# Performance work log

Measured on AMD Instinct MI355X. Metric: run time of the kernel, lower is better.

The kernel has to match this reference:

```python
import jax, jax.numpy as jnp
import numpy as np

D_OUT = 64  # out_embed_size, also the softmax scale base

def setup_inputs() -> dict:
    key = jax.random.key(0)
    kx, kk, kq, kv = jax.random.split(key, 4)
    B, T, C = 8, 2048, 768
    x = jax.random.normal(kx, (B, T, C), dtype=jnp.float32)
    # torch Linear weights are [out, in]; store as [in, out] for x @ W
    s = 1.0 / np.sqrt(C)
    Wk = jax.random.uniform(kk, (C, D_OUT), jnp.float32, -s, s)
    Wq = jax.random.uniform(kq, (C, D_OUT), jnp.float32, -s, s)
    Wv = jax.random.uniform(kv, (C, D_OUT), jnp.float32, -s, s)
    return {"x": x, "Wq": Wq, "Wk": Wk, "Wv": Wv}

def reference(x, Wq, Wk, Wv):
    B, T, C = x.shape
    q = x @ Wq  # [B,T,D]
    k = x @ Wk
    v = x @ Wv
    scale = D_OUT ** -0.5
    qk = jnp.einsum('btd,bsd->bts', q, k) * scale  # [B,T,T]
    causal = jnp.tril(jnp.ones((T, T), dtype=bool))
    qk = jnp.where(causal, qk, -jnp.inf)
    attn = jax.nn.softmax(qk, axis=-1)
    # dropout p=0.0 -> identity
    return jnp.einsum('bts,bsd->btd', attn, v)
```

## Files before the change

### kernel.cpp

```cpp
#include <hip/hip_runtime.h>
#include <hip/hip_bf16.h>

#define BB 8
#define TT 2048
#define CC 768
#define DD 64
#define BT (BB * TT)

typedef __attribute__((ext_vector_type(8))) short bf16x8;
typedef __attribute__((ext_vector_type(4))) float f32x4;

__device__ __forceinline__ unsigned short f2b(float f) {
  unsigned u = __builtin_bit_cast(unsigned, f);
  u += 0x7fffu + ((u >> 16) & 1u);
  return (unsigned short)(u >> 16);
}

__device__ __forceinline__ bf16x8 pack8(float4 a, float4 b) {
  unsigned short t[8] = {f2b(a.x), f2b(a.y), f2b(a.z), f2b(a.w),
                         f2b(b.x), f2b(b.y), f2b(b.z), f2b(b.w)};
  return *reinterpret_cast<bf16x8*>(t);
}

__device__ __forceinline__ void gl16(const void* g, void* l) {
  __builtin_amdgcn_global_load_lds(
      (const __attribute__((address_space(1))) unsigned int*)g,
      (__attribute__((address_space(3))) unsigned int*)l, 16, 0, 0);
}

__global__ __launch_bounds__(256) void wt_kernel(const float* __restrict__ Wq,
                                                 const float* __restrict__ Wk,
                                                 const float* __restrict__ Wv,
                                                 unsigned short* __restrict__ wt) {
  int tid = blockIdx.x * 256 + threadIdx.x;
  if (tid >= 192 * 96) return;
  int k0 = (tid % 96) * 8;
  int c = tid / 96;
  const float* W = (c < 64) ? Wq : (c < 128 ? Wk : Wv);
  int cc = c & 63;
  unsigned short t[8];
#pragma unroll
  for (int e = 0; e < 8; ++e) t[e] = f2b(W[(k0 + e) * 64 + cc]);
  *reinterpret_cast<bf16x8*>(&wt[c * 768 + k0]) = *reinterpret_cast<bf16x8*>(t);
}

__global__ __launch_bounds__(512, 2) void proj_kernel(const float* __restrict__ x,
                                                      const unsigned short* __restrict__ wt,
                                                      unsigned short* __restrict__ qws,
                                                      unsigned short* __restrict__ kws,
                                                      unsigned short* __restrict__ vtws) {
  __shared__ __align__(16) float xl[2][32 * 64];
  __shared__ __align__(16) unsigned short wl[2][192 * 64];

  const int tid = threadIdx.x;
  const int wv = tid >> 6;
  const int l = tid & 63;
  const int lo = l & 15, hi = l >> 4;
  const int rg = wv & 1;
  const int cq = wv >> 1;
  const int m0 = blockIdx.x * 32;

  const int xrow = tid >> 4;
  const int xcs = ((tid & 15) ^ (xrow & 7)) * 4;
  const float* xsrc = x + (size_t)(m0 + xrow) * 768 + xcs;
  const int xdst = (tid & ~63) * 4;

  f32x4 acc[3];
#pragma unroll
  for (int i = 0; i < 3; ++i) acc[i] = (f32x4){0.f, 0.f, 0.f, 0.f};

  auto stage = [&](int buf, int k0) {
    gl16(xsrc + k0, &xl[buf][xdst]);
#pragma unroll
    for (int it = 0; it < 3; ++it) {
      int ch = tid + it * 512;
      int row = ch >> 3;
      int c = ((ch & 7) ^ (row & 7)) * 8;
      gl16(wt + row * 768 + k0 + c, &wl[buf][(ch & ~63) * 8]);
    }
  };

  stage(0, 0);
  __syncthreads();

  const int arow = rg * 16 + lo;
  const int ax = arow & 7;
  int buf = 0;
#pragma unroll
  for (int step = 0; step < 12; ++step) {
    if (step < 11) stage(buf ^ 1, (step + 1) * 64);

    const float* xb = xl[buf];
    const unsigned short* wb = wl[buf];
    float4 a0 = *reinterpret_cast<const float4*>(&xb[arow * 64 + ((hi * 2 + 0) ^ ax) * 4]);
    float4 a1 = *reinterpret_cast<const float4*>(&xb[arow * 64 + ((hi * 2 + 1) ^ ax) * 4]);
    float4 a2 = *reinterpret_cast<const float4*>(&xb[arow * 64 + ((8 + hi * 2 + 0) ^ ax) * 4]);
    float4 a3 = *reinterpret_cast<const float4*>(&xb[arow * 64 + ((8 + hi * 2 + 1) ^ ax) * 4]);
    bf16x8 af0 = pack8(a0, a1);
    bf16x8 af1 = pack8(a2, a3);
#pragma unroll
    for (int ct = 0; ct < 3; ++ct) {
      int cr = cq * 48 + ct * 16 + lo;
      int cx = cr & 7;
      bf16x8 b0 = *reinterpret_cast<const bf16x8*>(&wb[cr * 64 + ((hi) ^ cx) * 8]);
      bf16x8 b1 = *reinterpret_cast<const bf16x8*>(&wb[cr * 64 + ((4 + hi) ^ cx) * 8]);
      acc[ct] = __builtin_amdgcn_mfma_f32_16x16x32_bf16(af0, b0, acc[ct], 0, 0, 0);
      acc[ct] = __builtin_amdgcn_mfma_f32_16x16x32_bf16(af1, b1, acc[ct], 0, 0, 0);
    }
    __syncthreads();
    buf ^= 1;
  }

  const float QS = 0.125f * 1.4426950408889634f;
#pragma unroll
  for (int ct = 0; ct < 3; ++ct) {
    const int c = cq * 48 + ct * 16 + lo;
    const int mat = c >> 6;
    const int cc = c & 63;
#pragma unroll
    for (int r = 0; r < 4; ++r) {
      const int m = m0 + rg * 16 + hi * 4 + r;
      float val = acc[ct][r];
      if (mat == 0) {
        qws[m * 64 + cc] = f2b(val * QS);
      } else if (mat == 1) {
        kws[m * 64 + cc] = f2b(val);
      } else {
        vtws[(size_t)((m >> 11) * 64 + cc) * 2048 + (m & 2047)] = f2b(val);
      }
    }
  }
}

__global__ __launch_bounds__(256, 2) void attn_kernel(const unsigned short* __restrict__ qws,
                                                      const unsigned short* __restrict__ kws,
                                                      const unsigned short* __restrict__ vtws,
                                                      float* __restrict__ out) {
  __shared__ __align__(16) unsigned short Kl[2][128 * 64];
  __shared__ __align__(16) unsigned short Vl[2][64 * 128];
  __shared__ __align__(16) unsigned short Pl[4][16 * 40];
  __shared__ float Obuf[16][68];
  __shared__ float Ssum[16];

  const int tid = threadIdx.x;
  const int s = tid >> 6;
  const int l = tid & 63;
  const int lo = l & 15, hi = l >> 4;
  const int b = blockIdx.x & 7;
  const int u0 = blockIdx.x >> 3;

  const unsigned short* qb = qws + (size_t)b * TT * DD;
  const unsigned short* kb = kws + (size_t)b * TT * DD;
  const unsigned short* vb = vtws + (size_t)b * DD * TT;
  unsigned short* Plw = &Pl[s][0];

  auto stage = [&](int buf, int kv0) {
#pragma unroll
    for (int it = 0; it < 4; ++it) {
      int ch = tid + it * 256;
      int kr = ch >> 3;
      int kc = ((ch & 7) ^ (kr & 7)) * 8;
      gl16(kb + (size_t)(kv0 + kr) * 64 + kc, &Kl[buf][(ch & ~63) * 8]);
      int vd = ch >> 4;
      int vc = ((ch & 15) ^ (vd & 7)) * 8;
      gl16(vb + (size_t)vd * 2048 + kv0 + vc, &Vl[buf][(ch & ~63) * 8]);
    }
  };

  for (int phase = 0; phase < 2; ++phase) {
    const int u = phase ? (127 - u0) : u0;
    const int t0 = u * 16;
    const int nt = (u >> 3) + 1;

    __syncthreads();
    for (int i = tid; i < 16 * 68; i += 256) (&Obuf[0][0])[i] = 0.f;
    if (tid < 16) Ssum[tid] = 0.f;

    bf16x8 qf0 = *reinterpret_cast<const bf16x8*>(&qb[(t0 + lo) * 64 + hi * 8]);
    bf16x8 qf1 = *reinterpret_cast<const bf16x8*>(&qb[(t0 + lo) * 64 + 32 + hi * 8]);

    f32x4 Oa[4];
#pragma unroll
    for (int n = 0; n < 4; ++n) Oa[n] = (f32x4){0.f, 0.f, 0.f, 0.f};
    float srow[4] = {0.f, 0.f, 0.f, 0.f};

    stage(0, 0);
    __syncthreads();

    int buf = 0;
    for (int j = 0; j < nt; ++j) {
      if (j + 1 < nt) stage(buf ^ 1, (j + 1) * 128);

      const unsigned short* Kb = &Kl[buf][0];
      const unsigned short* Vb = &Vl[buf][0];

      f32x4 S0 = (f32x4){0.f, 0.f, 0.f, 0.f};
      f32x4 S1 = (f32x4){0.f, 0.f, 0.f, 0.f};
      {
        int key = s * 32 + lo;
        int kx = key & 7;
        bf16x8 k0f = *reinterpret_cast<const bf16x8*>(&Kb[key * 64 + ((hi) ^ kx) * 8]);
        bf16x8 k1f = *reinterpret_cast<const bf16x8*>(&Kb[key * 64 + ((4 + hi) ^ kx) * 8]);
        S0 = __builtin_amdgcn_mfma_f32_16x16x32_bf16(qf0, k0f, S0, 0, 0, 0);
        S0 = __builtin_amdgcn_mfma_f32_16x16x32_bf16(qf1, k1f, S0, 0, 0, 0);
      }
      {
        int key = s * 32 + 16 + lo;
        int kx = key & 7;
        bf16x8 k0f = *reinterpret_cast<const bf16x8*>(&Kb[key * 64 + ((hi) ^ kx) * 8]);
        bf16x8 k1f = *reinterpret_cast<const bf16x8*>(&Kb[key * 64 + ((4 + hi) ^ kx) * 8]);
        S1 = __builtin_amdgcn_mfma_f32_16x16x32_bf16(qf0, k0f, S1, 0, 0, 0);
        S1 = __builtin_amdgcn_mfma_f32_16x16x32_bf16(qf1, k1f, S1, 0, 0, 0);
      }

      if (j == nt - 1) {
        const int kg0 = j * 128 + s * 32 + lo;
        const int kg1 = kg0 + 16;
#pragma unroll
        for (int r = 0; r < 4; ++r) {
          int qg = t0 + hi * 4 + r;
          if (kg0 > qg) S0[r] = -1e30f;
          if (kg1 > qg) S1[r] = -1e30f;
        }
      }

#pragma unroll
      for (int r = 0; r < 4; ++r) {
        float p0 = exp2f(S0[r]);
        float p1 = exp2f(S1[r]);
        srow[r] += p0 + p1;
        Plw[(hi * 4 + r) * 40 + lo] = f2b(p0);
        Plw[(hi * 4 + r) * 40 + 16 + lo] = f2b(p1);
      }
      bf16x8 pa = *reinterpret_cast<const bf16x8*>(&Plw[lo * 40 + hi * 8]);

#pragma unroll
      for (int n = 0; n < 4; ++n) {
        int d = n * 16 + lo;
        int dx = d & 7;
        bf16x8 vf = *reinterpret_cast<const bf16x8*>(&Vb[d * 128 + ((s * 4 + hi) ^ dx) * 8]);
        Oa[n] = __builtin_amdgcn_mfma_f32_16x16x32_bf16(pa, vf, Oa[n], 0, 0, 0);
      }

      __syncthreads();
      buf ^= 1;
    }

#pragma unroll
    for (int n = 0; n < 4; ++n)
#pragma unroll
      for (int r = 0; r < 4; ++r)
        atomicAdd(&Obuf[hi * 4 + r][n * 16 + lo], Oa[n][r]);
#pragma unroll
    for (int r = 0; r < 4; ++r) {
      float v = srow[r];
      v += __shfl_xor(v, 1);
      v += __shfl_xor(v, 2);
      v += __shfl_xor(v, 4);
      v += __shfl_xor(v, 8);
      if (lo == 0) atomicAdd(&Ssum[hi * 4 + r], v);
    }
    __syncthreads();

    {
      const int row = tid >> 4;
      const int c4 = (tid & 15) * 4;
      const float inv = 1.0f / Ssum[row];
      float4 o;
      o.x = Obuf[row][c4 + 0] * inv;
      o.y = Obuf[row][c4 + 1] * inv;
      o.z = Obuf[row][c4 + 2] * inv;
      o.w = Obuf[row][c4 + 3] * inv;
      *reinterpret_cast<float4*>(&out[((size_t)b * TT + t0 + row) * 64 + c4]) = o;
    }
  }
}

extern "C" void kernel_launch(void* const* d_in, const int* in_sizes, int n_in,
                              void* d_out, int out_size, void* d_ws, size_t ws_size,
                              hipStream_t stream) {
  const float* x = (const float*)d_in[0];
  const float* Wq = (const float*)d_in[1];
  const float* Wk = (const float*)d_in[2];
  const float* Wv = (const float*)d_in[3];
  float* out = (float*)d_out;

  char* ws = (char*)d_ws;
  unsigned short* qws = (unsigned short*)(ws);
  unsigned short* kws = (unsigned short*)(ws + (size_t)2 * 1024 * 1024);
  unsigned short* vtws = (unsigned short*)(ws + (size_t)4 * 1024 * 1024);
  unsigned short* wt = (unsigned short*)(ws + (size_t)6 * 1024 * 1024);

  hipLaunchKernelGGL(wt_kernel, dim3(72), dim3(256), 0, stream, Wq, Wk, Wv, wt);
  hipLaunchKernelGGL(proj_kernel, dim3(BT / 32), dim3(512), 0, stream, x, wt, qws, kws, vtws);
  hipLaunchKernelGGL(attn_kernel, dim3(512), dim3(256), 0, stream, qws, kws, vtws, out);
}
```

Baseline: 145.6 us.

## Merge attention phases into one pipelined loop with split barriers and wave priority

The attention kernel's two query-tile phases are fused into a single 17-iteration loop. K/V staging continues across the phase boundary, so the pipeline is not drained and refilled, and each phase keeps its own output and sum buffers. Both the projection and attention loops swap __syncthreads for explicit vmcnt waits plus raw s_barrier, so the next tile's loads stay in flight while compute proceeds. s_setprio is raised around the MFMA blocks. The hand-written waitcnt counts depend on an exact number of outstanding loads per thread, and a wrong count would let compute read stale LDS.

```diff
diff --git a/kernel.cpp b/kernel.cpp
--- a/kernel.cpp
+++ b/kernel.cpp
@@ -27,6 +27,13 @@
       (const __attribute__((address_space(1))) unsigned int*)g,
       (__attribute__((address_space(3))) unsigned int*)l, 16, 0, 0);
 }
+
+#define RAW_BAR()                                \
+  do {                                           \
+    asm volatile("" ::: "memory");               \
+    __builtin_amdgcn_s_barrier();                \
+    asm volatile("" ::: "memory");               \
+  } while (0)
 
 __global__ __launch_bounds__(256) void wt_kernel(const float* __restrict__ Wq,
                                                  const float* __restrict__ Wk,
@@ -81,14 +88,19 @@
   };
 
   stage(0, 0);
-  __syncthreads();
 
   const int arow = rg * 16 + lo;
   const int ax = arow & 7;
   int buf = 0;
-#pragma unroll
   for (int step = 0; step < 12; ++step) {
-    if (step < 11) stage(buf ^ 1, (step + 1) * 64);
+    if (step < 11) {
+      stage(buf ^ 1, (step + 1) * 64);
+      asm volatile("s_waitcnt vmcnt(4)" ::: "memory");
+    } else {
+      asm volatile("s_waitcnt vmcnt(0)" ::: "memory");
+    }
+    __builtin_amdgcn_s_barrier();
+    __builtin_amdgcn_sched_barrier(0);
 
     const float* xb = xl[buf];
     const unsigned short* wb = wl[buf];
@@ -98,6 +110,7 @@
     float4 a3 = *reinterpret_cast<const float4*>(&xb[arow * 64 + ((8 + hi * 2 + 1) ^ ax) * 4]);
     bf16x8 af0 = pack8(a0, a1);
     bf16x8 af1 = pack8(a2, a3);
+    __builtin_amdgcn_s_setprio(1);
 #pragma unroll
     for (int ct = 0; ct < 3; ++ct) {
       int cr = cq * 48 + ct * 16 + lo;
@@ -107,7 +120,8 @@
       acc[ct] = __builtin_amdgcn_mfma_f32_16x16x32_bf16(af0, b0, acc[ct], 0, 0, 0);
       acc[ct] = __builtin_amdgcn_mfma_f32_16x16x32_bf16(af1, b1, acc[ct], 0, 0, 0);
     }
-    __syncthreads();
+    __builtin_amdgcn_s_setprio(0);
+    RAW_BAR();
     buf ^= 1;
   }
 
@@ -139,8 +153,8 @@
   __shared__ __align__(16) unsigned short Kl[2][128 * 64];
   __shared__ __align__(16) unsigned short Vl[2][64 * 128];
   __shared__ __align__(16) unsigned short Pl[4][16 * 40];
-  __shared__ float Obuf[16][68];
-  __shared__ float Ssum[16];
+  __shared__ float Obuf[2][16][68];
+  __shared__ float Ssum[2][16];
 
   const int tid = threadIdx.x;
   const int s = tid >> 6;
@@ -149,10 +163,23 @@
   const int b = blockIdx.x & 7;
   const int u0 = blockIdx.x >> 3;
 
+  const int uA = u0, uB = 127 - u0;
+  const int t0A = uA * 16, t0B = uB * 16;
+  const int ntA = (uA >> 3) + 1;
+  const int ntot = 17;
+
   const unsigned short* qb = qws + (size_t)b * TT * DD;
   const unsigned short* kb = kws + (size_t)b * TT * DD;
   const unsigned short* vb = vtws + (size_t)b * DD * TT;
   unsigned short* Plw = &Pl[s][0];
+
+  for (int i = tid; i < 2 * 16 * 68; i += 256) (&Obuf[0][0][0])[i] = 0.f;
+  if (tid < 32) (&Ssum[0][0])[tid] = 0.f;
+
+  const bf16x8 qA0 = *reinterpret_cast<const bf16x8*>(&qb[(t0A + lo) * 64 + hi * 8]);
+  const bf16x8 qA1 = *reinterpret_cast<const bf16x8*>(&qb[(t0A + lo) * 64 + 32 + hi * 8]);
+  const bf16x8 qB0 = *reinterpret_cast<const bf16x8*>(&qb[(t0B + lo) * 64 + hi * 8]);
+  const bf16x8 qB1 = *reinterpret_cast<const bf16x8*>(&qb[(t0B + lo) * 64 + 32 + hi * 8]);
 
   auto stage = [&](int buf, int kv0) {
 #pragma unroll
@@ -167,110 +194,135 @@
     }
   };
 
-  for (int phase = 0; phase < 2; ++phase) {
-    const int u = phase ? (127 - u0) : u0;
-    const int t0 = u * 16;
-    const int nt = (u >> 3) + 1;
-
-    __syncthreads();
-    for (int i = tid; i < 16 * 68; i += 256) (&Obuf[0][0])[i] = 0.f;
-    if (tid < 16) Ssum[tid] = 0.f;
-
-    bf16x8 qf0 = *reinterpret_cast<const bf16x8*>(&qb[(t0 + lo) * 64 + hi * 8]);
-    bf16x8 qf1 = *reinterpret_cast<const bf16x8*>(&qb[(t0 + lo) * 64 + 32 + hi * 8]);
-
-    f32x4 Oa[4];
-#pragma unroll
-    for (int n = 0; n < 4; ++n) Oa[n] = (f32x4){0.f, 0.f, 0.f, 0.f};
-    float srow[4] = {0.f, 0.f, 0.f, 0.f};
-
-    stage(0, 0);
-    __syncthreads();
-
-    int buf = 0;
-    for (int j = 0; j < nt; ++j) {
-      if (j + 1 < nt) stage(buf ^ 1, (j + 1) * 128);
-
-      const unsigned short* Kb = &Kl[buf][0];
-      const unsigned short* Vb = &Vl[buf][0];
-
-      f32x4 S0 = (f32x4){0.f, 0.f, 0.f, 0.f};
-      f32x4 S1 = (f32x4){0.f, 0.f, 0.f, 0.f};
-      {
-        int key = s * 32 + lo;
-        int kx = key & 7;
-        bf16x8 k0f = *reinterpret_cast<const bf16x8*>(&Kb[key * 64 + ((hi) ^ kx) * 8]);
-        bf16x8 k1f = *reinterpret_cast<const bf16x8*>(&Kb[key * 64 + ((4 + hi) ^ kx) * 8]);
-        S0 = __builtin_amdgcn_mfma_f32_16x16x32_bf16(qf0, k0f, S0, 0, 0, 0);
-        S0 = __builtin_amdgcn_mfma_f32_16x16x32_bf16(qf1, k1f, S0, 0, 0, 0);
+  f32x4 Oa[4];
+#pragma unroll
+  for (int n = 0; n < 4; ++n) Oa[n] = (f32x4){0.f, 0.f, 0.f, 0.f};
+  float srow[4] = {0.f, 0.f, 0.f, 0.f};
+
+  stage(0, 0);
+
+  int buf = 0;
+  for (int j = 0; j < ntot; ++j) {
+    if (j + 1 < ntot) {
+      const int jn = j + 1;
+      stage(buf ^ 1, (jn < ntA ? jn : jn - ntA) * 128);
+      asm volatile("s_waitcnt vmcnt(8)" ::: "memory");
+    } else {
+      asm volatile("s_waitcnt vmcnt(0)" ::: "memory");
+    }
+    __builtin_amdgcn_s_barrier();
+    __builtin_amdgcn_sched_barrier(0);
+
+    const unsigned short* Kb = &Kl[buf][0];
+    const unsigned short* Vb = &Vl[buf][0];
+    const bool isA = (j < ntA);
+    const int t0 = isA ? t0A : t0B;
+    const bf16x8 qf0 = isA ? qA0 : qB0;
+    const bf16x8 qf1 = isA ? qA1 : qB1;
+
+    f32x4 S0 = (f32x4){0.f, 0.f, 0.f, 0.f};
+    f32x4 S1 = (f32x4){0.f, 0.f, 0.f, 0.f};
+    __builtin_amdgcn_s_setprio(1);
+    {
+      int key = s * 32 + lo;
+      int kx = key & 7;
+      bf16x8 k0f = *reinterpret_cast<const bf16x8*>(&Kb[key * 64 + ((hi) ^ kx) * 8]);
+      bf16x8 k1f = *reinterpret_cast<const bf16x8*>(&Kb[key * 64 + ((4 + hi) ^ kx) * 8]);
+      S0 = __builtin_amdgcn_mfma_f32_16x16x32_bf16(qf0, k0f, S0, 0, 0, 0);
+      S0 = __builtin_amdgcn_mfma_f32_16x16x32_bf16(qf1, k1f, S0, 0, 0, 0);
+    }
+    {
+      int key = s * 32 + 16 + lo;
+      int kx = key & 7;
+      bf16x8 k0f = *reinterpret_cast<const bf16x8*>(&Kb[key * 64 + ((hi) ^ kx) * 8]);
+      bf16x8 k1f = *reinterpret_cast<const bf16x8*>(&Kb[key * 64 + ((4 + hi) ^ kx) * 8]);
+      S1 = __builtin_amdgcn_mfma_f32_16x16x32_bf16(qf0, k0f, S1, 0, 0, 0);
+      S1 = __builtin_amdgcn_mfma_f32_16x16x32_bf16(qf1, k1f, S1, 0, 0, 0);
+    }
+    __builtin_amdgcn_s_setprio(0);
+
+    if (j == ntA - 1 || j == ntot - 1) {
+      const int kg0 = (isA ? j : j - ntA) * 128 + s * 32 + lo;
+#pragma unroll
+      for (int r = 0; r < 4; ++r) {
+        int qg = t0 + hi * 4 + r;
+        if (kg0 > qg) S0[r] = -1e30f;
+        if (kg0 + 16 > qg) S1[r] = -1e30f;
       }
-      {
-        int key = s * 32 + 16 + lo;
-        int kx = key & 7;
-        bf16x8 k0f = *reinterpret_cast<const bf16x8*>(&Kb[key * 64 + ((hi) ^ kx) * 8]);
-        bf16x8 k1f = *reinterpret_cast<const bf16x8*>(&Kb[key * 64 + ((4 + hi) ^ kx) * 8]);
-        S1 = __builtin_amdgcn_mfma_f32_16x16x32_bf16(qf0, k0f, S1, 0, 0, 0);
-        S1 = __builtin_amdgcn_mfma_f32_16x16x32_bf16(qf1, k1f, S1, 0, 0, 0);
+    }
+
+#pragma unroll
+    for (int r = 0; r < 4; ++r) {
+      float p0 = exp2f(S0[r]);
+      float p1 = exp2f(S1[r]);
+      srow[r] += p0 + p1;
+      Plw[(hi * 4 + r) * 40 + lo] = f2b(p0);
+      Plw[(hi * 4 + r) * 40 + 16 + lo] = f2b(p1);
+    }
+    bf16x8 pa = *reinterpret_cast<const bf16x8*>(&Plw[lo * 40 + hi * 8]);
+
+    __builtin_amdgcn_s_setprio(1);
+#pragma unroll
+    for (int n = 0; n < 4; ++n) {
+      int d = n * 16 + lo;
+      int dx = d & 7;
+      bf16x8 vf = *reinterpret_cast<const bf16x8*>(&Vb[d * 128 + ((s * 4 + hi) ^ dx) * 8]);
+      Oa[n] = __builtin_amdgcn_mfma_f32_16x16x32_bf16(pa, vf, Oa[n], 0, 0, 0);
+    }
+    __builtin_amdgcn_s_setprio(0);
+
+    if (j == ntA - 1) {
+#pragma unroll
+      for (int n = 0; n < 4; ++n)
+#pragma unroll
+        for (int r = 0; r < 4; ++r)
+          atomicAdd(&Obuf[0][hi * 4 + r][n * 16 + lo], Oa[n][r]);
+#pragma unroll
+      for (int r = 0; r < 4; ++r) {
+        float v = srow[r];
+        v += __shfl_xor(v, 1);
+        v += __shfl_xor(v, 2);
+        v += __shfl_xor(v, 4);
+        v += __shfl_xor(v, 8);
+        if (lo == 0) atomicAdd(&Ssum[0][hi * 4 + r], v);
+        srow[r] = 0.f;
       }
-
-      if (j == nt - 1) {
-        const int kg0 = j * 128 + s * 32 + lo;
-        const int kg1 = kg0 + 16;
-#pragma unroll
-        for (int r = 0; r < 4; ++r) {
-          int qg = t0 + hi * 4 + r;
-          if (kg0 > qg) S0[r] = -1e30f;
-          if (kg1 > qg) S1[r] = -1e30f;
-        }
-      }
-
-#pragma unroll
-      for (int r = 0; r < 4; ++r) {
-        float p0 = exp2f(S0[r]);
-        float p1 = exp2f(S1[r]);
-        srow[r] += p0 + p1;
-        Plw[(hi * 4 + r) * 40 + lo] = f2b(p0);
-        Plw[(hi * 4 + r) * 40 + 16 + lo] = f2b(p1);
-      }
-      bf16x8 pa = *reinterpret_cast<const bf16x8*>(&Plw[lo * 40 + hi * 8]);
-
-#pragma unroll
-      for (int n = 0; n < 4; ++n) {
-        int d = n * 16 + lo;
-        int dx = d & 7;
-        bf16x8 vf = *reinterpret_cast<const bf16x8*>(&Vb[d * 128 + ((s * 4 + hi) ^ dx) * 8]);
-        Oa[n] = __builtin_amdgcn_mfma_f32_16x16x32_bf16(pa, vf, Oa[n], 0, 0, 0);
-      }
-
-      __syncthreads();
-      buf ^= 1;
-    }
-
-#pragma unroll
-    for (int n = 0; n < 4; ++n)
-#pragma unroll
-      for (int r = 0; r < 4; ++r)
-        atomicAdd(&Obuf[hi * 4 + r][n * 16 + lo], Oa[n][r]);
-#pragma unroll
-    for (int r = 0; r < 4; ++r) {
-      float v = srow[r];
-      v += __shfl_xor(v, 1);
-      v += __shfl_xor(v, 2);
-      v += __shfl_xor(v, 4);
-      v += __shfl_xor(v, 8);
-      if (lo == 0) atomicAdd(&Ssum[hi * 4 + r], v);
-    }
-    __syncthreads();
-
-    {
-      const int row = tid >> 4;
-      const int c4 = (tid & 15) * 4;
-      const float inv = 1.0f / Ssum[row];
+#pragma unroll
+      for (int n = 0; n < 4; ++n) Oa[n] = (f32x4){0.f, 0.f, 0.f, 0.f};
+    }
+
+    RAW_BAR();
+    buf ^= 1;
+  }
+
+#pragma unroll
+  for (int n = 0; n < 4; ++n)
+#pragma unroll
+    for (int r = 0; r < 4; ++r)
+      atomicAdd(&Obuf[1][hi * 4 + r][n * 16 + lo], Oa[n][r]);
+#pragma unroll
+  for (int r = 0; r < 4; ++r) {
+    float v = srow[r];
+    v += __shfl_xor(v, 1);
+    v += __shfl_xor(v, 2);
+    v += __shfl_xor(v, 4);
+    v += __shfl_xor(v, 8);
+    if (lo == 0) atomicAdd(&Ssum[1][hi * 4 + r], v);
+  }
+  __syncthreads();
+
+  {
+    const int row = tid >> 4;
+    const int c4 = (tid & 15) * 4;
+#pragma unroll
+    for (int t = 0; t < 2; ++t) {
+      const int t0 = t ? t0B : t0A;
+      const float inv = 1.0f / Ssum[t][row];
       float4 o;
-      o.x = Obuf[row][c4 + 0] * inv;
-      o.y = Obuf[row][c4 + 1] * inv;
-      o.z = Obuf[row][c4 + 2] * inv;
-      o.w = Obuf[row][c4 + 3] * inv;
+      o.x = Obuf[t][row][c4 + 0] * inv;
+      o.y = Obuf[t][row][c4 + 1] * inv;
+      o.z = Obuf[t][row][c4 + 2] * inv;
+      o.w = Obuf[t][row][c4 + 3] * inv;
       *reinterpret_cast<float4*>(&out[((size_t)b * TT + t0 + row) * 64 + c4]) = o;
     }
   }
```

After: 145.2 us. About the same (-0.3%).
